# Kernel optimization log

Hardware: AMD Instinct MI355X
Metric: run time of the kernel (lower is better)

The kernel has to match this reference:

```python
import jax, jax.numpy as jnp
import numpy as np

D_MODEL, H, D_FF = 1024, 16, 4096
B, S = 2, 2048
EPS = 1e-05


def layer_norm(x, gamma, beta):
    # Matches torch: mean and UNBIASED std over last dim, scalar gamma/beta,
    # and eps added to std (not variance).
    mean = jnp.mean(x, axis=-1, keepdims=True)
    var = jnp.sum((x - mean) ** 2, axis=-1, keepdims=True) / (x.shape[-1] - 1)
    return gamma * (x - mean) / (jnp.sqrt(var) + EPS) + beta


def setup_inputs() -> dict:
    key = jax.random.key(0)
    ks = jax.random.split(key, 16)
    sd = 1.0 / np.sqrt(D_MODEL)
    sf = 1.0 / np.sqrt(D_FF)
    return {
        "x": jax.random.normal(ks[0], (B, S, D_MODEL), jnp.float32),
        "mask": jnp.ones((1, 1, S, S), jnp.int32),
        "wq": jax.random.uniform(ks[1], (D_MODEL, D_MODEL), jnp.float32, -sd, sd),
        "bq": jax.random.uniform(ks[2], (D_MODEL,), jnp.float32, -sd, sd),
        "wk": jax.random.uniform(ks[3], (D_MODEL, D_MODEL), jnp.float32, -sd, sd),
        "bk": jax.random.uniform(ks[4], (D_MODEL,), jnp.float32, -sd, sd),
        "wv": jax.random.uniform(ks[5], (D_MODEL, D_MODEL), jnp.float32, -sd, sd),
        "bv": jax.random.uniform(ks[6], (D_MODEL,), jnp.float32, -sd, sd),
        "wo": jax.random.uniform(ks[7], (D_MODEL, D_MODEL), jnp.float32, -sd, sd),
        "bo": jax.random.uniform(ks[8], (D_MODEL,), jnp.float32, -sd, sd),
        "w1": jax.random.uniform(ks[9], (D_FF, D_MODEL), jnp.float32, -sd, sd),
        "b1": jax.random.uniform(ks[10], (D_FF,), jnp.float32, -sd, sd),
        "w2": jax.random.uniform(ks[11], (D_MODEL, D_FF), jnp.float32, -sf, sf),
        "b2": jax.random.uniform(ks[12], (D_MODEL,), jnp.float32, -sf, sf),
        "gamma1": jnp.ones((1,), jnp.float32),
        "beta1": jnp.zeros((1,), jnp.float32),
        "gamma2": jnp.ones((1,), jnp.float32),
        "beta2": jnp.zeros((1,), jnp.float32),
    }


def reference(x, mask, wq, bq, wk, bk, wv, bv, wo, bo, w1, b1, w2, b2,
              gamma1, beta1, gamma2, beta2):
    d_k = D_MODEL // H

    # --- residual 1: pre-LN self-attention ---
    xn = layer_norm(x, gamma1, beta1)
    q = (xn @ wq.T + bq).reshape(B, S, H, d_k).transpose(0, 2, 1, 3)
    k = (xn @ wk.T + bk).reshape(B, S, H, d_k).transpose(0, 2, 1, 3)
    v = (xn @ wv.T + bv).reshape(B, S, H, d_k).transpose(0, 2, 1, 3)

    scores = jnp.einsum("bhqd,bhkd->bhqk", q, k) / jnp.sqrt(
        jnp.asarray(d_k, x.dtype))
    scores = jnp.where(mask == 0, jnp.asarray(-1e9, x.dtype), scores)
    attn = jax.nn.softmax(scores, axis=-1)
    ctx = jnp.einsum("bhqk,bhkd->bhqd", attn, v)
    ctx = ctx.transpose(0, 2, 1, 3).reshape(B, S, D_MODEL)
    x = x + (ctx @ wo.T + bo)

    # --- residual 2: pre-LN feed-forward ---
    xn = layer_norm(x, gamma2, beta2)
    h = jax.nn.relu(xn @ w1.T + b1)
    x = x + (h @ w2.T + b2)
    return x
```

## Files before the change

kernel.cpp:

```cpp
#include <hip/hip_runtime.h>


typedef __bf16 bf16_t;
typedef __attribute__((ext_vector_type(8))) __bf16 bf16x8;
typedef __attribute__((ext_vector_type(4))) __bf16 bf16x4;
typedef __attribute__((ext_vector_type(2))) __bf16 bf16x2;
typedef __attribute__((ext_vector_type(4))) float f32x4;
typedef __attribute__((ext_vector_type(16))) float f32x16;
typedef __attribute__((ext_vector_type(2))) unsigned uint32x2;
typedef __attribute__((ext_vector_type(4))) unsigned uint32x4;

#define MB (1024ull * 1024ull)
#define QSCALE 0.18033688011112043f

__device__ __forceinline__ void gload_lds16(const bf16_t* g, bf16_t* l) {
    __builtin_amdgcn_global_load_lds(
        (const __attribute__((address_space(1))) void*)g,
        (__attribute__((address_space(3))) void*)l, 16, 0, 0);
}

__device__ __forceinline__ int bswz(int row) { return ((row >> 1) & 3) << 3; }

__device__ __forceinline__ int swz(int row, int col) {
    return row * 64 + ((((col >> 3) ^ row) & 7) << 3) + (col & 7);
}

__device__ __forceinline__ unsigned cvtpk(float a, float b) {
    bf16x2 v = {(__bf16)a, (__bf16)b};
    return __builtin_bit_cast(unsigned, v);
}

__global__ __launch_bounds__(256) void cvt_all(
    const float* __restrict__ wq, const float* __restrict__ wk,
    const float* __restrict__ wv, const float* __restrict__ wo,
    const float* __restrict__ w1, const float* __restrict__ w2,
    bf16_t* __restrict__ wqkv, bf16_t* __restrict__ wob, bf16_t* __restrict__ w1b,
    bf16_t* __restrict__ w2b) {
    const int b = blockIdx.x, t = threadIdx.x;
    const float* in;
    bf16_t* out;
    int i;
    if (b < 1024) { in = wq; out = wqkv; i = b * 256 + t; }
    else if (b < 2048) { in = wk; out = wqkv + 1048576; i = (b - 1024) * 256 + t; }
    else if (b < 3072) { in = wv; out = wqkv + 2097152; i = (b - 2048) * 256 + t; }
    else if (b < 4096) { in = wo; out = wob; i = (b - 3072) * 256 + t; }
    else if (b < 8192) { in = w1; out = w1b; i = (b - 4096) * 256 + t; }
    else { in = w2; out = w2b; i = (b - 8192) * 256 + t; }
    float4 v = ((const float4*)in)[i];
    bf16x4 o = {(__bf16)v.x, (__bf16)v.y, (__bf16)v.z, (__bf16)v.w};
    ((bf16x4*)out)[i] = o;
}

__global__ __launch_bounds__(256) void ln_kernel(const float* __restrict__ x,
                                                 bf16_t* __restrict__ out,
                                                 const float* __restrict__ gamma,
                                                 const float* __restrict__ beta) {
    const int lane = threadIdx.x & 63;
    const int row = blockIdx.x * 4 + (threadIdx.x >> 6);
    const float* xr = x + (size_t)row * 1024;
    float4 v[4];
    float s = 0.f;
#pragma unroll
    for (int i = 0; i < 4; ++i) {
        v[i] = ((const float4*)xr)[i * 64 + lane];
        s += v[i].x + v[i].y + v[i].z + v[i].w;
    }
#pragma unroll
    for (int o = 32; o; o >>= 1) s += __shfl_xor(s, o);
    float mean = s * (1.f / 1024.f);
    float vs = 0.f;
#pragma unroll
    for (int i = 0; i < 4; ++i) {
        float a = v[i].x - mean, b = v[i].y - mean, c = v[i].z - mean, d = v[i].w - mean;
        vs += a * a + b * b + c * c + d * d;
    }
#pragma unroll
    for (int o = 32; o; o >>= 1) vs += __shfl_xor(vs, o);
    float inv = 1.f / (sqrtf(vs * (1.f / 1023.f)) + 1e-5f);
    float g = gamma[0] * inv, bb = beta[0];
    bf16_t* orow = out + (size_t)row * 1024;
#pragma unroll
    for (int i = 0; i < 4; ++i) {
        bf16x4 ov = {(__bf16)((v[i].x - mean) * g + bb), (__bf16)((v[i].y - mean) * g + bb),
                     (__bf16)((v[i].z - mean) * g + bb), (__bf16)((v[i].w - mean) * g + bb)};
        *(bf16x4*)(orow + (i * 64 + lane) * 4) = ov;
    }
}

template <int KERN>
__global__ __launch_bounds__(512, 2) void gemm256(
    const bf16_t* __restrict__ A, const bf16_t* __restrict__ Bw, int K,
    const float* __restrict__ bias0, const float* __restrict__ bias1,
    const float* __restrict__ bias2, void* __restrict__ o0, void* __restrict__ o1,
    void* __restrict__ o2) {
    __shared__ bf16_t L[4 * 16384];
    const int t = threadIdx.x, lane = t & 63, w = t >> 6;
    const int wm = w >> 2, wn = w & 3;
    const int l15 = lane & 15, l4 = lane >> 4;
    const int bm = blockIdx.x, bn = blockIdx.y;
    const int NT = K >> 5;
    const bf16_t* Ab = A + (size_t)bm * 256 * K;
    const bf16_t* Bb = Bw + (size_t)bn * 256 * K;
    const int srow = t >> 2, pcol = (t & 3) * 8;
    f32x4 acc[8][4] = {};

    auto stageA = [&](int tt) {
        bf16_t* s = L + (tt & 3) * 16384;
        const int kb = tt * 32;
#pragma unroll
        for (int i = 0; i < 2; ++i) {
            int row = i * 128 + srow;
            int lcol = pcol ^ bswz(row);
            gload_lds16(Ab + (size_t)row * K + kb + lcol, s + i * 4096 + t * 8);
        }
    };
    auto stageB = [&](int tt) {
        bf16_t* s = L + (tt & 3) * 16384 + 8192;
        const int kb = tt * 32;
#pragma unroll
        for (int i = 0; i < 2; ++i) {
            int row = i * 128 + srow;
            int lcol = pcol ^ bswz(row);
            gload_lds16(Bb + (size_t)row * K + kb + lcol, s + i * 4096 + t * 8);
        }
    };

    stageA(0); stageB(0); stageA(1); stageB(1); stageA(2); stageB(2);
    asm volatile("s_waitcnt vmcnt(8)" ::: "memory");
    __builtin_amdgcn_s_barrier();

    for (int tt = 0; tt < NT; ++tt) {
        bf16_t* s = L + (tt & 3) * 16384;
        bf16_t* sB = s + 8192;
        bf16x8 af[4], bfr[4];
#pragma unroll
        for (int m = 0; m < 4; ++m) {
            int row = wm * 128 + m * 16 + l15;
            af[m] = *(const bf16x8*)(s + row * 32 + ((l4 * 8) ^ bswz(row)));
        }
#pragma unroll
        for (int n = 0; n < 4; ++n) {
            int row = wn * 64 + n * 16 + l15;
            bfr[n] = *(const bf16x8*)(sB + row * 32 + ((l4 * 8) ^ bswz(row)));
        }
        if (tt + 3 < NT) stageA(tt + 3);
        __builtin_amdgcn_s_barrier();
        __builtin_amdgcn_s_setprio(1);
#pragma unroll
        for (int m = 0; m < 4; ++m)
#pragma unroll
            for (int n = 0; n < 4; ++n)
                acc[m][n] = __builtin_amdgcn_mfma_f32_16x16x32_bf16(af[m], bfr[n], acc[m][n],
                                                                   0, 0, 0);
        __builtin_amdgcn_s_setprio(0);
        __builtin_amdgcn_s_barrier();
#pragma unroll
        for (int m = 0; m < 4; ++m) {
            int row = wm * 128 + 64 + m * 16 + l15;
            af[m] = *(const bf16x8*)(s + row * 32 + ((l4 * 8) ^ bswz(row)));
        }
        if (tt + 3 < NT) stageB(tt + 3);
        __builtin_amdgcn_s_barrier();
        __builtin_amdgcn_s_setprio(1);
#pragma unroll
        for (int m = 0; m < 4; ++m)
#pragma unroll
            for (int n = 0; n < 4; ++n)
                acc[4 + m][n] = __builtin_amdgcn_mfma_f32_16x16x32_bf16(af[m], bfr[n],
                                                                       acc[4 + m][n], 0, 0, 0);
        __builtin_amdgcn_s_setprio(0);
        if (tt + 3 < NT)
            asm volatile("s_waitcnt vmcnt(8)" ::: "memory");
        else if (tt + 2 < NT)
            asm volatile("s_waitcnt vmcnt(4)" ::: "memory");
        else
            asm volatile("s_waitcnt vmcnt(0)" ::: "memory");
        __builtin_amdgcn_s_barrier();
    }

    if (KERN == 1) {
        const int colb = bn * 256 + wn * 64;
        float bb[4];
#pragma unroll
        for (int n = 0; n < 4; ++n) bb[n] = bias0[colb + n * 16 + l15];
#pragma unroll
        for (int m = 0; m < 8; ++m) {
            const int row0 = bm * 256 + wm * 128 + m * 16 + (l4 << 2);
#pragma unroll
            for (int n = 0; n < 4; ++n)
#pragma unroll
                for (int j = 0; j < 4; ++j) {
                    float v = acc[m][n][j] + bb[n];
                    ((bf16_t*)o0)[(size_t)(row0 + j) * 4096 + colb + n * 16 + l15] =
                        (bf16_t)(v > 0.f ? v : 0.f);
                }
        }
        return;
    }
    if (bn < 8) {
        const bool isq = bn < 4;
        const float* bias = isq ? bias0 : bias1;
        const int head = (bn & 3) * 4 + wn;
        const int b = (bm * 256) >> 11;
        const int srow0 = (bm * 256 + wm * 128) & 2047;
        bf16_t* dst = (bf16_t*)(isq ? o0 : o1) + ((size_t)(b * 16 + head) << 17);
        float bb[4];
#pragma unroll
        for (int n = 0; n < 4; ++n) bb[n] = bias[head * 64 + n * 16 + l15];
#pragma unroll
        for (int m = 0; m < 8; ++m)
#pragma unroll
            for (int n = 0; n < 4; ++n)
#pragma unroll
                for (int j = 0; j < 4; ++j) {
                    int srw = srow0 + m * 16 + (l4 << 2) + j;
                    float v = acc[m][n][j] + bb[n];
                    if (isq) v *= QSCALE;
                    dst[((size_t)srw << 6) + n * 16 + l15] = (bf16_t)v;
                }
    } else {
        const int head = (bn - 8) * 4 + wn;
        const int b = (bm * 256) >> 11;
        const int sbase = (bm * 256 + wm * 128) & 2047;
        bf16_t* P = L + w * 8192;
        float bb[4];
#pragma unroll
        for (int n = 0; n < 4; ++n) bb[n] = bias2[head * 64 + n * 16 + l15];
#pragma unroll
        for (int m = 0; m < 8; ++m)
#pragma unroll
            for (int n = 0; n < 4; ++n) {
                int d = n * 16 + l15;
                int sl = m * 16 + (l4 << 2);
                bf16x4 pk = {(__bf16)(acc[m][n][0] + bb[n]), (__bf16)(acc[m][n][1] + bb[n]),
                             (__bf16)(acc[m][n][2] + bb[n]), (__bf16)(acc[m][n][3] + bb[n])};
                *(bf16x4*)(P + d * 128 + (sl ^ ((d & 7) << 3))) = pk;
            }
#pragma unroll
        for (int p = 0; p < 16; ++p) {
            int id = p * 64 + lane;
            int d = id >> 4, c8 = (id & 15) * 8;
            bf16x8 vv = *(const bf16x8*)(P + d * 128 + (c8 ^ ((d & 7) << 3)));
            *(bf16x8*)((bf16_t*)o2 + (((size_t)(b * 16 + head) * 64 + d) << 11) + sbase + c8) =
                vv;
        }
    }
}

template <int SPLIT>
__global__ __launch_bounds__(256, 2) void gemm128sq(
    const bf16_t* __restrict__ A, const bf16_t* __restrict__ Bw, int stride, int Ks,
    const float* __restrict__ bias, const float* __restrict__ resid,
    void* __restrict__ o0, void* __restrict__ o1) {
    __shared__ bf16_t L[4 * 8192];
    const int t = threadIdx.x, lane = t & 63, w = t >> 6;
    const int wr = w >> 1, wc = w & 1;
    const int l15 = lane & 15, l4 = lane >> 4;
    const int bm = blockIdx.x, bn = blockIdx.y;
    const int NT = Ks >> 5;
    const size_t kofs = SPLIT ? (size_t)blockIdx.z * Ks : 0;
    const bf16_t* Ab = A + (size_t)bm * 128 * stride + kofs;
    const bf16_t* Bb = Bw + (size_t)bn * 128 * stride + kofs;
    const int srow = t >> 2, pcol = (t & 3) * 8;
    f32x4 acc[4][4] = {};

    auto STAGE = [&](int tt) {
        bf16_t* s = L + (tt & 3) * 8192;
        const int kb = tt * 32;
#pragma unroll
        for (int i = 0; i < 2; ++i) {
            int row = i * 64 + srow;
            int lcol = pcol ^ bswz(row);
            gload_lds16(Ab + (size_t)row * stride + kb + lcol, s + i * 2048 + t * 8);
            gload_lds16(Bb + (size_t)row * stride + kb + lcol, s + 4096 + i * 2048 + t * 8);
        }
    };

    STAGE(0); STAGE(1); STAGE(2);
    asm volatile("s_waitcnt vmcnt(8)" ::: "memory");
    __builtin_amdgcn_s_barrier();

    for (int tt = 0; tt < NT; ++tt) {
        bf16_t* s = L + (tt & 3) * 8192;
        bf16x8 af[4], bfr[4];
#pragma unroll
        for (int m = 0; m < 4; ++m) {
            int row = wr * 64 + m * 16 + l15;
            af[m] = *(const bf16x8*)(s + row * 32 + ((l4 * 8) ^ bswz(row)));
        }
#pragma unroll
        for (int n = 0; n < 4; ++n) {
            int row = wc * 64 + n * 16 + l15;
            bfr[n] = *(const bf16x8*)(s + 4096 + row * 32 + ((l4 * 8) ^ bswz(row)));
        }
        if (tt + 3 < NT) STAGE(tt + 3);
        __builtin_amdgcn_s_barrier();
        __builtin_amdgcn_s_setprio(1);
#pragma unroll
        for (int m = 0; m < 4; ++m)
#pragma unroll
            for (int n = 0; n < 4; ++n)
                acc[m][n] = __builtin_amdgcn_mfma_f32_16x16x32_bf16(af[m], bfr[n], acc[m][n],
                                                                   0, 0, 0);
        __builtin_amdgcn_s_setprio(0);
        if (tt + 3 < NT)
            asm volatile("s_waitcnt vmcnt(8)" ::: "memory");
        else if (tt + 2 < NT)
            asm volatile("s_waitcnt vmcnt(4)" ::: "memory");
        else
            asm volatile("s_waitcnt vmcnt(0)" ::: "memory");
        __builtin_amdgcn_s_barrier();
    }

#pragma unroll
    for (int m = 0; m < 4; ++m) {
        const int row0 = bm * 128 + wr * 64 + m * 16 + (l4 << 2);
#pragma unroll
        for (int n = 0; n < 4; ++n) {
            const int col = bn * 128 + wc * 64 + n * 16 + l15;
#pragma unroll
            for (int j = 0; j < 4; ++j) {
                const int row = row0 + j;
                if (SPLIT == 0) {
                    ((float*)o0)[(size_t)row * 1024 + col] =
                        resid[(size_t)row * 1024 + col] + acc[m][n][j] + bias[col];
                } else {
                    bf16_t* po = (bf16_t*)(blockIdx.z ? o1 : o0);
                    po[(size_t)row * 1024 + col] = (bf16_t)acc[m][n][j];
                }
            }
        }
    }
}

__global__ __launch_bounds__(256) void ffn2_combine(
    const bf16_t* __restrict__ p0, const bf16_t* __restrict__ p1,
    const float* __restrict__ resid, const float* __restrict__ bias,
    float* __restrict__ out) {
    int i = blockIdx.x * 256 + threadIdx.x;
    float4 r = ((const float4*)resid)[i];
    bf16x4 a = ((const bf16x4*)p0)[i];
    bf16x4 b = ((const bf16x4*)p1)[i];
    float4 bs = ((const float4*)bias)[i & 255];
    float4 o;
    o.x = r.x + (float)a.x + (float)b.x + bs.x;
    o.y = r.y + (float)a.y + (float)b.y + bs.y;
    o.z = r.z + (float)a.z + (float)b.z + bs.z;
    o.w = r.w + (float)a.w + (float)b.w + bs.w;
    ((float4*)out)[i] = o;
}

__global__ __launch_bounds__(256, 4) void attn_kernel(const bf16_t* __restrict__ q,
                                                      const bf16_t* __restrict__ k,
                                                      const bf16_t* __restrict__ vt,
                                                      bf16_t* __restrict__ ctx) {
    __shared__ bf16_t Kl[2][64 * 64];
    __shared__ bf16_t Vl[2][64 * 64];
    const int t = threadIdx.x, lane = t & 63, w = t >> 6;
    const int bid = blockIdx.x;
    const int xcd = bid & 7, j = bid >> 3;
    const int bh = xcd + ((j >> 4) << 3);
    const int qx = j & 15;
    const bf16_t* qg = q + (size_t)bh * 2048 * 64;
    const bf16_t* kg = k + (size_t)bh * 2048 * 64;
    const bf16_t* vg = vt + (size_t)bh * 64 * 2048;
    const int l31 = lane & 31, h = lane >> 5;
    const int rowl = w * 32 + l31;
    const int qrow = qx * 128 + rowl;
    const int prow = t >> 3, p = t & 7;
    const int sc = ((p ^ prow) & 7) * 8;

    bf16x8 qf[4];
#pragma unroll
    for (int kd = 0; kd < 4; ++kd)
        qf[kd] = *(const bf16x8*)(qg + (size_t)qrow * 64 + kd * 16 + h * 8);

    f32x16 o0 = {}, o1 = {};
    float mi = -1e30f, li = 0.f;

    auto STAGE = [&](int tt) {
        bf16_t* kd_ = Kl[tt & 1];
        bf16_t* vd_ = Vl[tt & 1];
        const int kb = tt * 64;
        gload_lds16(kg + (size_t)(kb + prow) * 64 + sc, kd_ + t * 8);
        gload_lds16(kg + (size_t)(kb + prow + 32) * 64 + sc, kd_ + 2048 + t * 8);
        gload_lds16(vg + (size_t)prow * 2048 + kb + sc, vd_ + t * 8);
        gload_lds16(vg + (size_t)(prow + 32) * 2048 + kb + sc, vd_ + 2048 + t * 8);
    };

    STAGE(0);
    const int NT = 32;
    for (int tt = 0; tt < NT; ++tt) {
        if (tt + 1 < NT) {
            STAGE(tt + 1);
            asm volatile("s_waitcnt vmcnt(4)" ::: "memory");
        } else {
            asm volatile("s_waitcnt vmcnt(0)" ::: "memory");
        }
        __builtin_amdgcn_s_barrier();
        const bf16_t* Kb = Kl[tt & 1];
        const bf16_t* Vb = Vl[tt & 1];
        f32x16 sT0 = {}, sT1 = {};
        __builtin_amdgcn_s_setprio(1);
#pragma unroll
        for (int kd = 0; kd < 4; ++kd) {
            bf16x8 ka0 = *(const bf16x8*)(Kb + swz(l31, kd * 16 + h * 8));
            bf16x8 ka1 = *(const bf16x8*)(Kb + swz(32 + l31, kd * 16 + h * 8));
            sT0 = __builtin_amdgcn_mfma_f32_32x32x16_bf16(ka0, qf[kd], sT0, 0, 0, 0);
            sT1 = __builtin_amdgcn_mfma_f32_32x32x16_bf16(ka1, qf[kd], sT1, 0, 0, 0);
        }
        __builtin_amdgcn_s_setprio(0);
        float pm[16];
#pragma unroll
        for (int i = 0; i < 16; ++i) pm[i] = fmaxf(sT0[i], sT1[i]);
#pragma unroll
        for (int st = 8; st; st >>= 1)
#pragma unroll
            for (int i = 0; i < st; ++i) pm[i] = fmaxf(pm[i], pm[i + st]);
        float mx = fmaxf(pm[0], __shfl_xor(pm[0], 32));
        if (!__all(mx <= mi + 8.f)) {
            float mn = fmaxf(mi, mx);
            float al = __builtin_amdgcn_exp2f(mi - mn);
            mi = mn;
            li *= al;
            o0 *= al;
            o1 *= al;
        }
        f32x16 e0, e1;
#pragma unroll
        for (int i = 0; i < 16; ++i) e0[i] = __builtin_amdgcn_exp2f(sT0[i] - mi);
#pragma unroll
        for (int i = 0; i < 16; ++i) e1[i] = __builtin_amdgcn_exp2f(sT1[i] - mi);
        float ps[16];
#pragma unroll
        for (int i = 0; i < 16; ++i) ps[i] = e0[i] + e1[i];
#pragma unroll
        for (int st = 8; st; st >>= 1)
#pragma unroll
            for (int i = 0; i < st; ++i) ps[i] += ps[i + st];
        li += ps[0] + __shfl_xor(ps[0], 32);
        bf16x8 pa[4];
#pragma unroll
        for (int kd = 0; kd < 4; ++kd) {
            const f32x16& e = (kd < 2) ? e0 : e1;
            const int R0l = 8 * (kd & 1);
            const int R0h = R0l + 4;
            unsigned U0 = cvtpk(e[R0l + 0], e[R0l + 1]);
            unsigned V0 = cvtpk(e[R0l + 2], e[R0l + 3]);
            unsigned U1 = cvtpk(e[R0h + 0], e[R0h + 1]);
            unsigned V1 = cvtpk(e[R0h + 2], e[R0h + 3]);
            uint32x2 ru = __builtin_amdgcn_permlane32_swap(U0, U1, false, false);
            uint32x2 rv = __builtin_amdgcn_permlane32_swap(V0, V1, false, false);
            uint32x4 pw = {ru.x, rv.x, ru.y, rv.y};
            pa[kd] = __builtin_bit_cast(bf16x8, pw);
        }
        __builtin_amdgcn_s_setprio(1);
#pragma unroll
        for (int kd = 0; kd < 4; ++kd) {
            bf16x8 va0 = *(const bf16x8*)(Vb + swz(l31, kd * 16 + h * 8));
            bf16x8 va1 = *(const bf16x8*)(Vb + swz(32 + l31, kd * 16 + h * 8));
            o0 = __builtin_amdgcn_mfma_f32_32x32x16_bf16(va0, pa[kd], o0, 0, 0, 0);
            o1 = __builtin_amdgcn_mfma_f32_32x32x16_bf16(va1, pa[kd], o1, 0, 0, 0);
        }
        __builtin_amdgcn_s_setprio(0);
        __builtin_amdgcn_s_barrier();
    }
    float inv = 1.f / li;
    size_t base = ((size_t)(bh >> 4) * 2048 + qrow) * 1024 + (bh & 15) * 64;
#pragma unroll
    for (int g = 0; g < 4; ++g) {
        bf16x4 ov0 = {(__bf16)(o0[4 * g + 0] * inv), (__bf16)(o0[4 * g + 1] * inv),
                      (__bf16)(o0[4 * g + 2] * inv), (__bf16)(o0[4 * g + 3] * inv)};
        *(bf16x4*)(ctx + base + 8 * g + 4 * h) = ov0;
        bf16x4 ov1 = {(__bf16)(o1[4 * g + 0] * inv), (__bf16)(o1[4 * g + 1] * inv),
                      (__bf16)(o1[4 * g + 2] * inv), (__bf16)(o1[4 * g + 3] * inv)};
        *(bf16x4*)(ctx + base + 32 + 8 * g + 4 * h) = ov1;
    }
}

extern "C" void kernel_launch(void* const* d_in, const int* in_sizes, int n_in,
                              void* d_out, int out_size, void* d_ws, size_t ws_size,
                              hipStream_t stream) {
    const float* x = (const float*)d_in[0];
    const float* wq = (const float*)d_in[2];
    const float* bq = (const float*)d_in[3];
    const float* wk = (const float*)d_in[4];
    const float* bk = (const float*)d_in[5];
    const float* wv = (const float*)d_in[6];
    const float* bv = (const float*)d_in[7];
    const float* wo = (const float*)d_in[8];
    const float* bo = (const float*)d_in[9];
    const float* w1 = (const float*)d_in[10];
    const float* b1 = (const float*)d_in[11];
    const float* w2 = (const float*)d_in[12];
    const float* b2 = (const float*)d_in[13];
    const float* gamma1 = (const float*)d_in[14];
    const float* beta1 = (const float*)d_in[15];
    const float* gamma2 = (const float*)d_in[16];
    const float* beta2 = (const float*)d_in[17];

    char* ws = (char*)d_ws;
    bf16_t* wqkv = (bf16_t*)(ws + 0);
    bf16_t* wob = (bf16_t*)(ws + 6 * MB);
    bf16_t* w1b = (bf16_t*)(ws + 8 * MB);
    bf16_t* w2b = (bf16_t*)(ws + 16 * MB);
    bf16_t* xnb = (bf16_t*)(ws + 24 * MB);
    bf16_t* qb = (bf16_t*)(ws + 32 * MB);
    bf16_t* kb = (bf16_t*)(ws + 40 * MB);
    bf16_t* vtb = (bf16_t*)(ws + 48 * MB);
    bf16_t* ctxb = (bf16_t*)(ws + 56 * MB);
    float* x1 = (float*)(ws + 64 * MB);
    bf16_t* hb = (bf16_t*)(ws + 32 * MB);
    bf16_t* p0 = (bf16_t*)(ws + 0);
    bf16_t* p1 = (bf16_t*)(ws + 24 * MB);

    cvt_all<<<12288, 256, 0, stream>>>(wq, wk, wv, wo, w1, w2, wqkv, wob, w1b, w2b);

    ln_kernel<<<1024, 256, 0, stream>>>(x, xnb, gamma1, beta1);
    gemm256<0><<<dim3(16, 12), 512, 0, stream>>>(xnb, wqkv, 1024, bq, bk, bv, qb, kb, vtb);
    attn_kernel<<<512, 256, 0, stream>>>(qb, kb, vtb, ctxb);
    gemm128sq<0><<<dim3(32, 8), 256, 0, stream>>>(ctxb, wob, 1024, 1024, bo, x, x1, nullptr);
    ln_kernel<<<1024, 256, 0, stream>>>(x1, xnb, gamma2, beta2);
    gemm256<1><<<dim3(16, 16), 512, 0, stream>>>(xnb, w1b, 1024, b1, nullptr, nullptr, hb,
                                                 nullptr, nullptr);
    gemm128sq<1><<<dim3(32, 8, 2), 256, 0, stream>>>(hb, w2b, 4096, 2048, nullptr, nullptr,
                                                     p0, p1);
    ffn2_combine<<<4096, 256, 0, stream>>>(p0, p1, x1, b2, (float*)d_out);
}
```

Measured before the change: 217.7 us.

## Double KV tile to 128 and prefetch through registers in attention

The attention kernel now processes 128 keys per iteration instead of 64, halving the loop count and the number of barriers. The double-buffered direct global-to-LDS loads are replaced by register prefetch: the next tile is read into registers during compute and written into a single LDS buffer after a barrier. This needs a new wider swizzle for V and lowers the launch-bounds occupancy hint from 4 to 2 blocks per CU, trading occupancy and register pressure for fewer synchronisations and larger MFMA batches.

New measurement: 213.2 us. 1.02x faster.

```diff
diff --git a/kernel.cpp b/kernel.cpp
--- a/kernel.cpp
+++ b/kernel.cpp
@@ -23,6 +23,10 @@
 
 __device__ __forceinline__ int swz(int row, int col) {
     return row * 64 + ((((col >> 3) ^ row) & 7) << 3) + (col & 7);
+}
+
+__device__ __forceinline__ int swzV(int row, int col) {
+    return row * 128 + ((((col >> 3) ^ row) & 15) << 3) + (col & 7);
 }
 
 __device__ __forceinline__ unsigned cvtpk(float a, float b) {
@@ -350,12 +354,12 @@
     ((float4*)out)[i] = o;
 }
 
-__global__ __launch_bounds__(256, 4) void attn_kernel(const bf16_t* __restrict__ q,
+__global__ __launch_bounds__(256, 2) void attn_kernel(const bf16_t* __restrict__ q,
                                                       const bf16_t* __restrict__ k,
                                                       const bf16_t* __restrict__ vt,
                                                       bf16_t* __restrict__ ctx) {
-    __shared__ bf16_t Kl[2][64 * 64];
-    __shared__ bf16_t Vl[2][64 * 64];
+    __shared__ bf16_t Kl[128 * 64];
+    __shared__ bf16_t Vl[64 * 128];
     const int t = threadIdx.x, lane = t & 63, w = t >> 6;
     const int bid = blockIdx.x;
     const int xcd = bid & 7, j = bid >> 3;
@@ -367,8 +371,8 @@
     const int l31 = lane & 31, h = lane >> 5;
     const int rowl = w * 32 + l31;
     const int qrow = qx * 128 + rowl;
-    const int prow = t >> 3, p = t & 7;
-    const int sc = ((p ^ prow) & 7) * 8;
+    const int kprow = t >> 3, kp8 = (t & 7) * 8;
+    const int vrow = t >> 2, vc = t & 3;
 
     bf16x8 qf[4];
 #pragma unroll
@@ -378,41 +382,43 @@
     f32x16 o0 = {}, o1 = {};
     float mi = -1e30f, li = 0.f;
 
-    auto STAGE = [&](int tt) {
-        bf16_t* kd_ = Kl[tt & 1];
-        bf16_t* vd_ = Vl[tt & 1];
-        const int kb = tt * 64;
-        gload_lds16(kg + (size_t)(kb + prow) * 64 + sc, kd_ + t * 8);
-        gload_lds16(kg + (size_t)(kb + prow + 32) * 64 + sc, kd_ + 2048 + t * 8);
-        gload_lds16(vg + (size_t)prow * 2048 + kb + sc, vd_ + t * 8);
-        gload_lds16(vg + (size_t)(prow + 32) * 2048 + kb + sc, vd_ + 2048 + t * 8);
-    };
-
-    STAGE(0);
-    const int NT = 32;
+    {
+#pragma unroll
+        for (int i = 0; i < 4; ++i) {
+            bf16x8 kv = *(const bf16x8*)(kg + (size_t)(kprow + 32 * i) * 64 + kp8);
+            *(bf16x8*)(Kl + swz(kprow + 32 * i, kp8)) = kv;
+            bf16x8 vv = *(const bf16x8*)(vg + (size_t)vrow * 2048 + (vc + 4 * i) * 8);
+            *(bf16x8*)(Vl + swzV(vrow, (vc + 4 * i) * 8)) = vv;
+        }
+    }
+
+    const int NT = 16;
     for (int tt = 0; tt < NT; ++tt) {
-        if (tt + 1 < NT) {
-            STAGE(tt + 1);
-            asm volatile("s_waitcnt vmcnt(4)" ::: "memory");
-        } else {
-            asm volatile("s_waitcnt vmcnt(0)" ::: "memory");
-        }
-        __builtin_amdgcn_s_barrier();
-        const bf16_t* Kb = Kl[tt & 1];
-        const bf16_t* Vb = Vl[tt & 1];
-        f32x16 sT0 = {}, sT1 = {};
+        __syncthreads();
+        bf16x8 kr[4], vr[4];
+        const bool more = (tt + 1) < NT;
+        if (more) {
+            const int kb = (tt + 1) * 128;
+#pragma unroll
+            for (int i = 0; i < 4; ++i) {
+                kr[i] = *(const bf16x8*)(kg + (size_t)(kb + kprow + 32 * i) * 64 + kp8);
+                vr[i] = *(const bf16x8*)(vg + (size_t)vrow * 2048 + kb + (vc + 4 * i) * 8);
+            }
+        }
+        f32x16 sT[4] = {};
         __builtin_amdgcn_s_setprio(1);
 #pragma unroll
-        for (int kd = 0; kd < 4; ++kd) {
-            bf16x8 ka0 = *(const bf16x8*)(Kb + swz(l31, kd * 16 + h * 8));
-            bf16x8 ka1 = *(const bf16x8*)(Kb + swz(32 + l31, kd * 16 + h * 8));
-            sT0 = __builtin_amdgcn_mfma_f32_32x32x16_bf16(ka0, qf[kd], sT0, 0, 0, 0);
-            sT1 = __builtin_amdgcn_mfma_f32_32x32x16_bf16(ka1, qf[kd], sT1, 0, 0, 0);
-        }
+        for (int kb = 0; kb < 4; ++kb)
+#pragma unroll
+            for (int kd = 0; kd < 4; ++kd) {
+                bf16x8 ka = *(const bf16x8*)(Kl + swz(kb * 32 + l31, kd * 16 + h * 8));
+                sT[kb] = __builtin_amdgcn_mfma_f32_32x32x16_bf16(ka, qf[kd], sT[kb], 0, 0, 0);
+            }
         __builtin_amdgcn_s_setprio(0);
         float pm[16];
 #pragma unroll
-        for (int i = 0; i < 16; ++i) pm[i] = fmaxf(sT0[i], sT1[i]);
+        for (int i = 0; i < 16; ++i)
+            pm[i] = fmaxf(fmaxf(sT[0][i], sT[1][i]), fmaxf(sT[2][i], sT[3][i]));
 #pragma unroll
         for (int st = 8; st; st >>= 1)
 #pragma unroll
@@ -426,23 +432,23 @@
             o0 *= al;
             o1 *= al;
         }
-        f32x16 e0, e1;
-#pragma unroll
-        for (int i = 0; i < 16; ++i) e0[i] = __builtin_amdgcn_exp2f(sT0[i] - mi);
-#pragma unroll
-        for (int i = 0; i < 16; ++i) e1[i] = __builtin_amdgcn_exp2f(sT1[i] - mi);
+#pragma unroll
+        for (int kb = 0; kb < 4; ++kb)
+#pragma unroll
+            for (int i = 0; i < 16; ++i) sT[kb][i] = __builtin_amdgcn_exp2f(sT[kb][i] - mi);
         float ps[16];
 #pragma unroll
-        for (int i = 0; i < 16; ++i) ps[i] = e0[i] + e1[i];
+        for (int i = 0; i < 16; ++i)
+            ps[i] = (sT[0][i] + sT[1][i]) + (sT[2][i] + sT[3][i]);
 #pragma unroll
         for (int st = 8; st; st >>= 1)
 #pragma unroll
             for (int i = 0; i < st; ++i) ps[i] += ps[i + st];
         li += ps[0] + __shfl_xor(ps[0], 32);
-        bf16x8 pa[4];
-#pragma unroll
-        for (int kd = 0; kd < 4; ++kd) {
-            const f32x16& e = (kd < 2) ? e0 : e1;
+        bf16x8 pa[8];
+#pragma unroll
+        for (int kd = 0; kd < 8; ++kd) {
+            const f32x16& e = sT[kd >> 1];
             const int R0l = 8 * (kd & 1);
             const int R0h = R0l + 4;
             unsigned U0 = cvtpk(e[R0l + 0], e[R0l + 1]);
@@ -456,14 +462,21 @@
         }
         __builtin_amdgcn_s_setprio(1);
 #pragma unroll
-        for (int kd = 0; kd < 4; ++kd) {
-            bf16x8 va0 = *(const bf16x8*)(Vb + swz(l31, kd * 16 + h * 8));
-            bf16x8 va1 = *(const bf16x8*)(Vb + swz(32 + l31, kd * 16 + h * 8));
+        for (int kd = 0; kd < 8; ++kd) {
+            bf16x8 va0 = *(const bf16x8*)(Vl + swzV(l31, kd * 16 + h * 8));
+            bf16x8 va1 = *(const bf16x8*)(Vl + swzV(32 + l31, kd * 16 + h * 8));
             o0 = __builtin_amdgcn_mfma_f32_32x32x16_bf16(va0, pa[kd], o0, 0, 0, 0);
             o1 = __builtin_amdgcn_mfma_f32_32x32x16_bf16(va1, pa[kd], o1, 0, 0, 0);
         }
         __builtin_amdgcn_s_setprio(0);
-        __builtin_amdgcn_s_barrier();
+        __syncthreads();
+        if (more) {
+#pragma unroll
+            for (int i = 0; i < 4; ++i) {
+                *(bf16x8*)(Kl + swz(kprow + 32 * i, kp8)) = kr[i];
+                *(bf16x8*)(Vl + swzV(vrow, (vc + 4 * i) * 8)) = vr[i];
+            }
+        }
     }
     float inv = 1.f / li;
     size_t base = ((size_t)(bh >> 4) * 2048 + qrow) * 1024 + (bh & 15) * 64;
```

## Fuse first layernorm into weight-cast kernel and software-pipeline attention loop

Applied to the files above, without the earlier changes.

Merges the first LayerNorm into the weight-conversion kernel so one launch is dropped. The attention kernel stops using direct global-to-LDS loads and instead prefetches the next K/V tile into registers, then writes it to LDS after compute. Softmax and PV for tile t-1 now run after QK^T for tile t, so exp and MFMA work can overlap. Launch bounds are lowered to 2 blocks per SM, which leaves room for the extra registers but may reduce occupancy.

After: 215.4 us. Within noise of the previous version (-1.1%).

```diff
diff --git a/kernel.cpp b/kernel.cpp
--- a/kernel.cpp
+++ b/kernel.cpp
@@ -30,25 +30,59 @@
     return __builtin_bit_cast(unsigned, v);
 }
 
-__global__ __launch_bounds__(256) void cvt_all(
+__global__ __launch_bounds__(256) void cvt_ln(
     const float* __restrict__ wq, const float* __restrict__ wk,
     const float* __restrict__ wv, const float* __restrict__ wo,
     const float* __restrict__ w1, const float* __restrict__ w2,
     bf16_t* __restrict__ wqkv, bf16_t* __restrict__ wob, bf16_t* __restrict__ w1b,
-    bf16_t* __restrict__ w2b) {
+    bf16_t* __restrict__ w2b, const float* __restrict__ x, bf16_t* __restrict__ xn,
+    const float* __restrict__ gamma, const float* __restrict__ beta) {
     const int b = blockIdx.x, t = threadIdx.x;
-    const float* in;
-    bf16_t* out;
-    int i;
-    if (b < 1024) { in = wq; out = wqkv; i = b * 256 + t; }
-    else if (b < 2048) { in = wk; out = wqkv + 1048576; i = (b - 1024) * 256 + t; }
-    else if (b < 3072) { in = wv; out = wqkv + 2097152; i = (b - 2048) * 256 + t; }
-    else if (b < 4096) { in = wo; out = wob; i = (b - 3072) * 256 + t; }
-    else if (b < 8192) { in = w1; out = w1b; i = (b - 4096) * 256 + t; }
-    else { in = w2; out = w2b; i = (b - 8192) * 256 + t; }
-    float4 v = ((const float4*)in)[i];
-    bf16x4 o = {(__bf16)v.x, (__bf16)v.y, (__bf16)v.z, (__bf16)v.w};
-    ((bf16x4*)out)[i] = o;
+    if (b < 12288) {
+        const float* in;
+        bf16_t* out;
+        int i;
+        if (b < 1024) { in = wq; out = wqkv; i = b * 256 + t; }
+        else if (b < 2048) { in = wk; out = wqkv + 1048576; i = (b - 1024) * 256 + t; }
+        else if (b < 3072) { in = wv; out = wqkv + 2097152; i = (b - 2048) * 256 + t; }
+        else if (b < 4096) { in = wo; out = wob; i = (b - 3072) * 256 + t; }
+        else if (b < 8192) { in = w1; out = w1b; i = (b - 4096) * 256 + t; }
+        else { in = w2; out = w2b; i = (b - 8192) * 256 + t; }
+        float4 v = ((const float4*)in)[i];
+        bf16x4 o = {(__bf16)v.x, (__bf16)v.y, (__bf16)v.z, (__bf16)v.w};
+        ((bf16x4*)out)[i] = o;
+        return;
+    }
+    const int lane = t & 63;
+    const int row = (b - 12288) * 4 + (t >> 6);
+    const float* xr = x + (size_t)row * 1024;
+    float4 v[4];
+    float s = 0.f;
+#pragma unroll
+    for (int i = 0; i < 4; ++i) {
+        v[i] = ((const float4*)xr)[i * 64 + lane];
+        s += v[i].x + v[i].y + v[i].z + v[i].w;
+    }
+#pragma unroll
+    for (int o = 32; o; o >>= 1) s += __shfl_xor(s, o);
+    float mean = s * (1.f / 1024.f);
+    float vs = 0.f;
+#pragma unroll
+    for (int i = 0; i < 4; ++i) {
+        float a = v[i].x - mean, bb2 = v[i].y - mean, c = v[i].z - mean, d = v[i].w - mean;
+        vs += a * a + bb2 * bb2 + c * c + d * d;
+    }
+#pragma unroll
+    for (int o = 32; o; o >>= 1) vs += __shfl_xor(vs, o);
+    float inv = 1.f / (sqrtf(vs * (1.f / 1023.f)) + 1e-5f);
+    float g = gamma[0] * inv, bb = beta[0];
+    bf16_t* orow = xn + (size_t)row * 1024;
+#pragma unroll
+    for (int i = 0; i < 4; ++i) {
+        bf16x4 ov = {(__bf16)((v[i].x - mean) * g + bb), (__bf16)((v[i].y - mean) * g + bb),
+                     (__bf16)((v[i].z - mean) * g + bb), (__bf16)((v[i].w - mean) * g + bb)};
+        *(bf16x4*)(orow + (i * 64 + lane) * 4) = ov;
+    }
 }
 
 __global__ __launch_bounds__(256) void ln_kernel(const float* __restrict__ x,
@@ -350,7 +384,7 @@
     ((float4*)out)[i] = o;
 }
 
-__global__ __launch_bounds__(256, 4) void attn_kernel(const bf16_t* __restrict__ q,
+__global__ __launch_bounds__(256, 2) void attn_kernel(const bf16_t* __restrict__ q,
                                                       const bf16_t* __restrict__ k,
                                                       const bf16_t* __restrict__ vt,
                                                       bf16_t* __restrict__ ctx) {
@@ -364,11 +398,9 @@
     const bf16_t* qg = q + (size_t)bh * 2048 * 64;
     const bf16_t* kg = k + (size_t)bh * 2048 * 64;
     const bf16_t* vg = vt + (size_t)bh * 64 * 2048;
+    const int r = t >> 3, c8 = (t & 7) * 8;
     const int l31 = lane & 31, h = lane >> 5;
-    const int rowl = w * 32 + l31;
-    const int qrow = qx * 128 + rowl;
-    const int prow = t >> 3, p = t & 7;
-    const int sc = ((p ^ prow) & 7) * 8;
+    const int qrow = qx * 128 + w * 32 + l31;
 
     bf16x8 qf[4];
 #pragma unroll
@@ -377,42 +409,12 @@
 
     f32x16 o0 = {}, o1 = {};
     float mi = -1e30f, li = 0.f;
-
-    auto STAGE = [&](int tt) {
-        bf16_t* kd_ = Kl[tt & 1];
-        bf16_t* vd_ = Vl[tt & 1];
-        const int kb = tt * 64;
-        gload_lds16(kg + (size_t)(kb + prow) * 64 + sc, kd_ + t * 8);
-        gload_lds16(kg + (size_t)(kb + prow + 32) * 64 + sc, kd_ + 2048 + t * 8);
-        gload_lds16(vg + (size_t)prow * 2048 + kb + sc, vd_ + t * 8);
-        gload_lds16(vg + (size_t)(prow + 32) * 2048 + kb + sc, vd_ + 2048 + t * 8);
-    };
-
-    STAGE(0);
-    const int NT = 32;
-    for (int tt = 0; tt < NT; ++tt) {
-        if (tt + 1 < NT) {
-            STAGE(tt + 1);
-            asm volatile("s_waitcnt vmcnt(4)" ::: "memory");
-        } else {
-            asm volatile("s_waitcnt vmcnt(0)" ::: "memory");
-        }
-        __builtin_amdgcn_s_barrier();
-        const bf16_t* Kb = Kl[tt & 1];
-        const bf16_t* Vb = Vl[tt & 1];
-        f32x16 sT0 = {}, sT1 = {};
-        __builtin_amdgcn_s_setprio(1);
-#pragma unroll
-        for (int kd = 0; kd < 4; ++kd) {
-            bf16x8 ka0 = *(const bf16x8*)(Kb + swz(l31, kd * 16 + h * 8));
-            bf16x8 ka1 = *(const bf16x8*)(Kb + swz(32 + l31, kd * 16 + h * 8));
-            sT0 = __builtin_amdgcn_mfma_f32_32x32x16_bf16(ka0, qf[kd], sT0, 0, 0, 0);
-            sT1 = __builtin_amdgcn_mfma_f32_32x32x16_bf16(ka1, qf[kd], sT1, 0, 0, 0);
-        }
-        __builtin_amdgcn_s_setprio(0);
+    f32x16 p0, p1;
+
+    auto SMPV = [&](f32x16& e0, f32x16& e1, const bf16_t* Vb) {
         float pm[16];
 #pragma unroll
-        for (int i = 0; i < 16; ++i) pm[i] = fmaxf(sT0[i], sT1[i]);
+        for (int i = 0; i < 16; ++i) pm[i] = fmaxf(e0[i], e1[i]);
 #pragma unroll
         for (int st = 8; st; st >>= 1)
 #pragma unroll
@@ -426,11 +428,10 @@
             o0 *= al;
             o1 *= al;
         }
-        f32x16 e0, e1;
-#pragma unroll
-        for (int i = 0; i < 16; ++i) e0[i] = __builtin_amdgcn_exp2f(sT0[i] - mi);
-#pragma unroll
-        for (int i = 0; i < 16; ++i) e1[i] = __builtin_amdgcn_exp2f(sT1[i] - mi);
+#pragma unroll
+        for (int i = 0; i < 16; ++i) e0[i] = __builtin_amdgcn_exp2f(e0[i] - mi);
+#pragma unroll
+        for (int i = 0; i < 16; ++i) e1[i] = __builtin_amdgcn_exp2f(e1[i] - mi);
         float ps[16];
 #pragma unroll
         for (int i = 0; i < 16; ++i) ps[i] = e0[i] + e1[i];
@@ -463,8 +464,58 @@
             o1 = __builtin_amdgcn_mfma_f32_32x32x16_bf16(va1, pa[kd], o1, 0, 0, 0);
         }
         __builtin_amdgcn_s_setprio(0);
-        __builtin_amdgcn_s_barrier();
-    }
+    };
+
+    {
+        bf16x8 k0 = *(const bf16x8*)(kg + (size_t)r * 64 + c8);
+        bf16x8 k1 = *(const bf16x8*)(kg + (size_t)(r + 32) * 64 + c8);
+        bf16x8 v0 = *(const bf16x8*)(vg + (size_t)r * 2048 + c8);
+        bf16x8 v1 = *(const bf16x8*)(vg + (size_t)(r + 32) * 2048 + c8);
+        *(bf16x8*)(&Kl[0][swz(r, c8)]) = k0;
+        *(bf16x8*)(&Kl[0][swz(r + 32, c8)]) = k1;
+        *(bf16x8*)(&Vl[0][swz(r, c8)]) = v0;
+        *(bf16x8*)(&Vl[0][swz(r + 32, c8)]) = v1;
+    }
+    __syncthreads();
+
+    const int NT = 32;
+    for (int tt = 0; tt < NT; ++tt) {
+        bf16x8 k0, k1, v0, v1;
+        const bool more = (tt + 1) < NT;
+        if (more) {
+            const int kb = (tt + 1) * 64;
+            k0 = *(const bf16x8*)(kg + (size_t)(kb + r) * 64 + c8);
+            k1 = *(const bf16x8*)(kg + (size_t)(kb + r + 32) * 64 + c8);
+            v0 = *(const bf16x8*)(vg + (size_t)r * 2048 + kb + c8);
+            v1 = *(const bf16x8*)(vg + (size_t)(r + 32) * 2048 + kb + c8);
+        }
+        const bf16_t* Kb = Kl[tt & 1];
+        f32x16 sT0 = {}, sT1 = {};
+        __builtin_amdgcn_s_setprio(1);
+#pragma unroll
+        for (int kd = 0; kd < 4; ++kd) {
+            bf16x8 ka0 = *(const bf16x8*)(Kb + swz(l31, kd * 16 + h * 8));
+            bf16x8 ka1 = *(const bf16x8*)(Kb + swz(32 + l31, kd * 16 + h * 8));
+            sT0 = __builtin_amdgcn_mfma_f32_32x32x16_bf16(ka0, qf[kd], sT0, 0, 0, 0);
+            sT1 = __builtin_amdgcn_mfma_f32_32x32x16_bf16(ka1, qf[kd], sT1, 0, 0, 0);
+        }
+        __builtin_amdgcn_s_setprio(0);
+        if (tt > 0) SMPV(p0, p1, Vl[(tt - 1) & 1]);
+        p0 = sT0;
+        p1 = sT1;
+        __syncthreads();
+        if (more) {
+            bf16_t* kd_ = Kl[(tt + 1) & 1];
+            bf16_t* vd_ = Vl[(tt + 1) & 1];
+            *(bf16x8*)(&kd_[swz(r, c8)]) = k0;
+            *(bf16x8*)(&kd_[swz(r + 32, c8)]) = k1;
+            *(bf16x8*)(&vd_[swz(r, c8)]) = v0;
+            *(bf16x8*)(&vd_[swz(r + 32, c8)]) = v1;
+        }
+        __syncthreads();
+    }
+    SMPV(p0, p1, Vl[1]);
+
     float inv = 1.f / li;
     size_t base = ((size_t)(bh >> 4) * 2048 + qrow) * 1024 + (bh & 15) * 64;
 #pragma unroll
@@ -514,9 +565,8 @@
     bf16_t* p0 = (bf16_t*)(ws + 0);
     bf16_t* p1 = (bf16_t*)(ws + 24 * MB);
 
-    cvt_all<<<12288, 256, 0, stream>>>(wq, wk, wv, wo, w1, w2, wqkv, wob, w1b, w2b);
-
-    ln_kernel<<<1024, 256, 0, stream>>>(x, xnb, gamma1, beta1);
+    cvt_ln<<<13312, 256, 0, stream>>>(wq, wk, wv, wo, w1, w2, wqkv, wob, w1b, w2b, x, xnb,
+                                      gamma1, beta1);
     gemm256<0><<<dim3(16, 12), 512, 0, stream>>>(xnb, wqkv, 1024, bq, bk, bv, qb, kb, vtb);
     attn_kernel<<<512, 256, 0, stream>>>(qb, kb, vtb, ctxb);
     gemm128sq<0><<<dim3(32, 8), 256, 0, stream>>>(ctxb, wob, 1024, 1024, bo, x, x1, nullptr);
```
